# Performance work log

Measured on AMD Instinct MI355X. Metric: run time of the kernel, lower is better.

## Reference

```python
import jax, jax.numpy as jnp
import numpy as np

B, N, INDIM = 512, 200, 200
D1, D2, D3 = 32, 32, 8
RATIO = 0.5
K1 = int(np.ceil(RATIO * N))    # 100 nodes kept after pool1
K2 = int(np.ceil(RATIO * K1))   # 50 nodes kept after pool2
BN_EPS = 1e-5
NEG = -1e9


def setup_inputs() -> dict:
    key = jax.random.key(0)
    ks = jax.random.split(key, 16)
    x = jax.random.normal(ks[0], (B, N, INDIM), jnp.float32)
    u = jax.random.uniform(ks[1], (B, N, N), jnp.float32)
    ut = jnp.triu(jnp.where(u > 0.9, u, 0.0), 1)
    adj = ut + jnp.swapaxes(ut, 1, 2)
    g = lambda i, shape: jax.random.normal(ks[i], shape, jnp.float32) * 0.1
    return dict(
        x=x, adj=adj,
        W1=g(2, (INDIM, D1)), a1s=g(3, (D1,)), a1d=g(4, (D1,)), b1=jnp.zeros((D1,), jnp.float32),
        W2=g(5, (D1, D2)), a2s=g(6, (D2,)), a2d=g(7, (D2,)), b2=jnp.zeros((D2,), jnp.float32),
        pw1=g(8, (D1,)), pw2=g(9, (D2,)),
        fc1_w=g(10, ((D1 + D2) * 2, D2)), fc1_b=jnp.zeros((D2,), jnp.float32),
        fc2_w=g(11, (D2, D3)), fc2_b=jnp.zeros((D3,), jnp.float32),
        fc3_w=g(12, (D3, 2)), fc3_b=jnp.zeros((2,), jnp.float32),
        bn4_g=jnp.ones((D2,), jnp.float32), bn4_b=jnp.zeros((D2,), jnp.float32),
        bn5_g=jnp.ones((D3,), jnp.float32), bn5_b=jnp.zeros((D3,), jnp.float32))


def _gat(x, mask, W, a_s, a_d, b):
    # PyG GATConv (heads=1): alpha_ij = softmax_j LeakyReLU(a_d.h_i + a_s.h_j) over in-neighbors j (self-loops added)
    h = jnp.einsum('bnf,fd->bnd', x, W)
    es = h @ a_s                    # [B,n] source term
    ed = h @ a_d                    # [B,n] dest term
    m = mask | jnp.eye(mask.shape[1], dtype=bool)
    logits = jax.nn.leaky_relu(ed[:, :, None] + es[:, None, :], 0.2)
    alpha = jax.nn.softmax(jnp.where(m, logits, NEG), axis=-1)   # [B,n,n]
    return jnp.einsum('bij,bjd->bid', alpha, h) + b


def _topk(x, adj_w, w, k):
    # TopKPooling(multiplier=1, nonlinearity=sigmoid): score = sigmoid(x.w/||w||)
    score = jax.nn.sigmoid((x @ w) / (jnp.linalg.norm(w) + 1e-16))   # [B,n]
    vals, idx = jax.lax.top_k(score, k)                              # perm sorted desc, as PyG
    xk = jnp.take_along_axis(x, idx[:, :, None], axis=1) * vals[:, :, None]
    ak = jnp.take_along_axis(jnp.take_along_axis(adj_w, idx[:, :, None], axis=1), idx[:, None, :], axis=2)
    return xk, ak, vals


def _bn(z, g, b):
    # eval-mode BatchNorm1d: running_mean=0, running_var=1
    return g * z / jnp.sqrt(1.0 + BN_EPS) + b


def reference(x, adj, W1, a1s, a1d, b1, W2, a2s, a2d, b2, pw1, pw2,
              fc1_w, fc1_b, fc2_w, fc2_b, fc3_w, fc3_b, bn4_g, bn4_b, bn5_g, bn5_b):
    h = _gat(x, adj > 0, W1, a1s, a1d, b1)
    h, aw, s1 = _topk(h, adj, pw1, K1)
    x1 = jnp.concatenate([h.max(axis=1), h.mean(axis=1)], axis=1)    # [B, 64]
    # augment_adj: add self-loops, spspmm (A+I)@(A+I), remove self-loops
    eye = jnp.eye(K1, dtype=aw.dtype)
    a2 = jnp.einsum('bij,bjk->bik', aw + eye, aw + eye) * (1.0 - eye)
    h = _gat(h, a2 != 0, W2, a2s, a2d, b2)
    h, _, s2 = _topk(h, a2, pw2, K2)
    x2 = jnp.concatenate([h.max(axis=1), h.mean(axis=1)], axis=1)    # [B, 64]
    z = jnp.concatenate([x1, x2], axis=1)                            # [B, 128]
    z = _bn(jax.nn.relu(z @ fc1_w + fc1_b), bn4_g, bn4_b)            # dropout: eval -> identity
    z = _bn(jax.nn.relu(z @ fc2_w + fc2_b), bn5_g, bn5_b)
    logp = jax.nn.log_softmax(z @ fc3_w + fc3_b, axis=-1)            # [B, 2]
    return logp, s1, s2
```

## Files before the change

### kernel.cpp

```cpp
#include <hip/hip_runtime.h>
#include <math.h>

#define N_   200
#define B_   512
#define K1_  100
#define K2_  50

#define S1_OFF 1024
#define S2_OFF 52224

#define WS_H    0u
#define WS_ES   13107200u
#define WS_ED   13516800u
#define WS_BITS 13926400u

__device__ __forceinline__ float lrelu(float v) { return v > 0.f ? v : 0.2f * v; }
__device__ __forceinline__ float sigm(float v)  { return 1.f / (1.f + __expf(-v)); }

__device__ __forceinline__ void bitonic_desc(float* key, int* idx, int n, int t) {
  for (int k = 2; k <= n; k <<= 1) {
    for (int j = k >> 1; j > 0; j >>= 1) {
      __syncthreads();
      int ixj = t ^ j;
      if (t < n && ixj > t) {
        float a = key[t], c = key[ixj];
        int ia = idx[t], ic = idx[ixj];
        bool gt = (a > c) || (a == c && ia < ic);
        if (((t & k) == 0) ? !gt : gt) {
          key[t] = c; key[ixj] = a; idx[t] = ic; idx[ixj] = ia;
        }
      }
    }
  }
  __syncthreads();
}

__global__ __launch_bounds__(128) void prep(
    const float* __restrict__ x, const float* __restrict__ adj,
    const float* __restrict__ W1, const float* __restrict__ a1s,
    const float* __restrict__ a1d,
    float* __restrict__ hg, float* __restrict__ esg, float* __restrict__ edg,
    unsigned* __restrict__ bitsg)
{
  const int t = threadIdx.x;
  const int blk = blockIdx.x;
  if (blk < 800) {
    const int r = blk * 128 + t;
    const float* xr = x + (size_t)r * 200;
    float acc[32];
    #pragma unroll
    for (int d = 0; d < 32; ++d) acc[d] = 0.f;
    for (int k4 = 0; k4 < 50; ++k4) {
      float4 xv = *(const float4*)(xr + k4 * 4);
      #pragma unroll
      for (int kk = 0; kk < 4; ++kk) {
        float xs = (&xv.x)[kk];
        const float* wr = W1 + (k4 * 4 + kk) * 32;
        #pragma unroll
        for (int d = 0; d < 32; ++d) acc[d] += xs * wr[d];
      }
    }
    float es = 0.f, ed = 0.f;
    #pragma unroll
    for (int d = 0; d < 32; ++d) { es += acc[d] * a1s[d]; ed += acc[d] * a1d[d]; }
    esg[r] = es; edg[r] = ed;
    float4* hg4 = (float4*)(hg + (size_t)r * 32);
    #pragma unroll
    for (int q = 0; q < 8; ++q)
      hg4[q] = make_float4(acc[q*4], acc[q*4+1], acc[q*4+2], acc[q*4+3]);
  } else {
    const int wg = (blk - 800) * 128 + t;
    const int row = wg / 7;
    const int w = wg - row * 7;
    const float* p = adj + (size_t)row * 200 + w * 32;
    unsigned m = 0u;
    const int lim = (w < 6) ? 32 : 8;
    for (int e = 0; e < lim; e += 4) {
      float4 v = *(const float4*)(p + e);
      m |= (unsigned)(v.x > 0.f) << e;
      m |= (unsigned)(v.y > 0.f) << (e + 1);
      m |= (unsigned)(v.z > 0.f) << (e + 2);
      m |= (unsigned)(v.w > 0.f) << (e + 3);
    }
    bitsg[wg] = m;
  }
}

__global__ __launch_bounds__(256) void gnn_main(
    const float* __restrict__ hg, const float* __restrict__ esg,
    const float* __restrict__ edg, const unsigned* __restrict__ bitsg,
    const float* __restrict__ b1, const float* __restrict__ W2g,
    const float* __restrict__ a2s, const float* __restrict__ a2d,
    const float* __restrict__ b2,
    const float* __restrict__ pw1, const float* __restrict__ pw2,
    const float* __restrict__ fc1w, const float* __restrict__ fc1b,
    const float* __restrict__ fc2w, const float* __restrict__ fc2b,
    const float* __restrict__ fc3w, const float* __restrict__ fc3b,
    const float* __restrict__ bn4g, const float* __restrict__ bn4b,
    const float* __restrict__ bn5g, const float* __restrict__ bn5b,
    float* __restrict__ out)
{
  __shared__ __align__(16) char smem[50592];
  float*    sH    = (float*)smem;
  unsigned* sBITS = (unsigned*)(smem + 25600);
  float*    sW2   = (float*)(smem + 25600);
  float*    sXK   = (float*)(smem + 31200);
  float*    sES   = (float*)(smem + 44000);
  float*    sED   = (float*)(smem + 44800);
  float*    sKey  = (float*)(smem + 45600);
  int*      sIdx  = (int*)(smem + 46624);
  int*      sInv  = (int*)(smem + 46624);
  int*      sSel  = (int*)(smem + 47648);
  float*    sVal  = (float*)(smem + 48048);
  float*    sXV   = (float*)(smem + 48448);
  float*    sRed  = (float*)(smem + 48960);
  unsigned* sMask2= (unsigned*)(smem + 48992);

  const int t = threadIdx.x;
  const int b = blockIdx.x;

  {
    const float4* hsrc = (const float4*)(hg + (size_t)b * 6400);
    float4* hdst = (float4*)sH;
    for (int i = t; i < 1600; i += 256) hdst[i] = hsrc[i];
    if (t < 50) {
      ((float4*)sES)[t] = ((const float4*)(esg + b * 200))[t];
      ((float4*)sED)[t] = ((const float4*)(edg + b * 200))[t];
    }
    const uint4* bsrc = (const uint4*)(bitsg + b * 1400);
    uint4* bdst = (uint4*)sBITS;
    for (int i = t; i < 350; i += 256) bdst[i] = bsrc[i];
  }
  __syncthreads();

  {
    float v = (t < N_) ? sES[t] : -3.0e38f;
    #pragma unroll
    for (int off = 1; off < 64; off <<= 1) v = fmaxf(v, __shfl_xor(v, off, 64));
    if ((t & 63) == 0) sRed[t >> 6] = v;
  }
  __syncthreads();
  const float esmax = fmaxf(fmaxf(sRed[0], sRed[1]), fmaxf(sRed[2], sRed[3]));

  const int wv = t >> 6, lane = t & 63;
  const int dg = lane >> 4, rg = lane & 15;
  float h1v[4][8]; float ssum1[4]; float edv1[4], Lv1[4];
  int rowc1[4]; bool val1[4];
  float b1c[8];
  *(float4*)&b1c[0] = *(const float4*)(b1 + dg * 8);
  *(float4*)&b1c[4] = *(const float4*)(b1 + dg * 8 + 4);
  {
    const int rbase = wv * 50;
    #pragma unroll
    for (int rr = 0; rr < 4; ++rr) {
      int rl = rg + 16 * rr;
      val1[rr] = rl < 50;
      rowc1[rr] = val1[rr] ? (rbase + rl) : 0;
      edv1[rr] = sED[rowc1[rr]];
      Lv1[rr]  = lrelu(edv1[rr] + esmax);
      ssum1[rr] = 0.f;
      #pragma unroll
      for (int u = 0; u < 8; ++u) h1v[rr][u] = 0.f;
    }
    for (int jw = 0; jw < 7; ++jw) {
      unsigned mw[4];
      #pragma unroll
      for (int rr = 0; rr < 4; ++rr) {
        mw[rr] = val1[rr] ? sBITS[rowc1[rr] * 7 + jw] : 0u;
        if (val1[rr] && (rowc1[rr] >> 5) == jw) mw[rr] |= 1u << (rowc1[rr] & 31);
      }
      const int cnt = (jw < 6) ? 32 : 8;
      for (int jj4 = 0; jj4 < cnt; jj4 += 4) {
        float4 esv = *(const float4*)&sES[jw * 32 + jj4];
        #pragma unroll
        for (int u = 0; u < 4; ++u) {
          int jj = jj4 + u;
          int j = jw * 32 + jj;
          float esj = (&esv.x)[u];
          float4 h0 = *(const float4*)&sH[j * 32 + dg * 8];
          float4 h1x = *(const float4*)&sH[j * 32 + dg * 8 + 4];
          #pragma unroll
          for (int rr = 0; rr < 4; ++rr) {
            float w = ((mw[rr] >> jj) & 1u) ? __expf(lrelu(edv1[rr] + esj) - Lv1[rr]) : 0.f;
            ssum1[rr] += w;
            h1v[rr][0] += w * h0.x;  h1v[rr][1] += w * h0.y;
            h1v[rr][2] += w * h0.z;  h1v[rr][3] += w * h0.w;
            h1v[rr][4] += w * h1x.x; h1v[rr][5] += w * h1x.y;
            h1v[rr][6] += w * h1x.z; h1v[rr][7] += w * h1x.w;
          }
        }
      }
    }
    #pragma unroll
    for (int rr = 0; rr < 4; ++rr) {
      float inv = 1.f / ssum1[rr];
      #pragma unroll
      for (int u = 0; u < 8; ++u) h1v[rr][u] = h1v[rr][u] * inv + b1c[u];
    }
  }

  {
    float npw = 0.f;
    #pragma unroll
    for (int d = 0; d < 32; ++d) npw += pw1[d] * pw1[d];
    npw = sqrtf(npw) + 1e-16f;
    float pwc[8];
    *(float4*)&pwc[0] = *(const float4*)(pw1 + dg * 8);
    *(float4*)&pwc[4] = *(const float4*)(pw1 + dg * 8 + 4);
    sKey[t] = -1.f; sIdx[t] = t;
    __syncthreads();
    #pragma unroll
    for (int rr = 0; rr < 4; ++rr) {
      float p = 0.f;
      #pragma unroll
      for (int u = 0; u < 8; ++u) p += h1v[rr][u] * pwc[u];
      p += __shfl_xor(p, 16, 64);
      p += __shfl_xor(p, 32, 64);
      if (dg == 0 && val1[rr]) sKey[rowc1[rr]] = sigm(p / npw);
    }
  }
  bitonic_desc(sKey, sIdx, 256, t);
  if (t < K1_) {
    out[S1_OFF + b * K1_ + t] = sKey[t];
    sVal[t] = sKey[t]; sSel[t] = sIdx[t];
  }
  __syncthreads();
  if (t < 200) sInv[t] = -1;
  __syncthreads();
  if (t < K1_) sInv[sSel[t]] = t;
  __syncthreads();
  #pragma unroll
  for (int rr = 0; rr < 4; ++rr) {
    if (val1[rr]) {
      int rk = sInv[rowc1[rr]];
      if (rk >= 0) {
        float vm = sVal[rk];
        float4 o0 = make_float4(h1v[rr][0]*vm, h1v[rr][1]*vm, h1v[rr][2]*vm, h1v[rr][3]*vm);
        float4 o1 = make_float4(h1v[rr][4]*vm, h1v[rr][5]*vm, h1v[rr][6]*vm, h1v[rr][7]*vm);
        *(float4*)&sXK[rk * 32 + dg * 8]     = o0;
        *(float4*)&sXK[rk * 32 + dg * 8 + 4] = o1;
      }
    }
  }
  __syncthreads();

  if (t < 32) {
    float m = -3.0e38f, s = 0.f;
    for (int r = 0; r < K1_; ++r) { float v = sXK[r * 32 + t]; m = fmaxf(m, v); s += v; }
    sXV[t] = m; sXV[32 + t] = s / 100.f;
  }

  if (t < K1_) {
    int gi = sSel[t];
    unsigned bt[7];
    #pragma unroll
    for (int w = 0; w < 7; ++w) bt[w] = sBITS[gi * 7 + w];
    #pragma unroll
    for (int w = 0; w < 4; ++w) {
      unsigned m = 0;
      const int lim = (w < 3) ? 32 : 4;
      for (int jj = 0; jj < lim; ++jj) {
        int j = w * 32 + jj;
        int gj = sSel[j];
        unsigned bit = (bt[gj >> 5] >> (gj & 31)) & 1u;
        if (j == t) bit = 1u;
        m |= bit << jj;
      }
      sMask2[t * 4 + w] = m;
    }
  }
  __syncthreads();
  {
    unsigned pr0 = 0, pr1 = 0, pr2 = 0, pr3 = 0;
    unsigned ow0 = 0, ow1 = 0, ow2 = 0, ow3 = 0;
    if (t < K1_) {
      ow0 = sMask2[t * 4 + 0]; ow1 = sMask2[t * 4 + 1];
      ow2 = sMask2[t * 4 + 2]; ow3 = sMask2[t * 4 + 3];
    }
    for (int k = 0; k < K1_; ++k) {
      uint4 mk = *(const uint4*)&sMask2[k * 4];
      unsigned bit = (k < 32) ? (ow0 >> k) : (k < 64) ? (ow1 >> (k - 32))
                   : (k < 96) ? (ow2 >> (k - 64)) : (ow3 >> (k - 96));
      unsigned sel = (bit & 1u) ? 0xFFFFFFFFu : 0u;
      pr0 |= mk.x & sel; pr1 |= mk.y & sel; pr2 |= mk.z & sel; pr3 |= mk.w & sel;
    }
    __syncthreads();
    if (t < K1_) {
      sMask2[t * 4 + 0] = pr0; sMask2[t * 4 + 1] = pr1;
      sMask2[t * 4 + 2] = pr2; sMask2[t * 4 + 3] = pr3;
    }
  }
  __syncthreads();

  for (int i = t; i < 1024; i += 256) sW2[i] = W2g[i];
  __syncthreads();
  if (t < K1_) {
    float acc[32];
    #pragma unroll
    for (int d = 0; d < 32; ++d) acc[d] = 0.f;
    const float4* xk4 = (const float4*)(sXK + t * 32);
    for (int k4 = 0; k4 < 8; ++k4) {
      float4 xv = xk4[k4];
      #pragma unroll
      for (int kk = 0; kk < 4; ++kk) {
        float xs = (&xv.x)[kk];
        const float* wr = &sW2[(k4 * 4 + kk) * 32];
        #pragma unroll
        for (int d = 0; d < 32; ++d) acc[d] += xs * wr[d];
      }
    }
    float es = 0.f, ed = 0.f;
    #pragma unroll
    for (int d = 0; d < 32; ++d) { es += acc[d] * a2s[d]; ed += acc[d] * a2d[d]; }
    sES[t] = es; sED[t] = ed;
    #pragma unroll
    for (int d = 0; d < 32; d += 4)
      *(float4*)&sH[t * 32 + d] = make_float4(acc[d], acc[d+1], acc[d+2], acc[d+3]);
  }
  __syncthreads();
  {
    float v = (t < K1_) ? sES[t] : -3.0e38f;
    #pragma unroll
    for (int off = 1; off < 64; off <<= 1) v = fmaxf(v, __shfl_xor(v, off, 64));
    if ((t & 63) == 0) sRed[t >> 6] = v;
  }
  __syncthreads();
  const float esm2 = fmaxf(fmaxf(sRed[0], sRed[1]), fmaxf(sRed[2], sRed[3]));

  float h2v[2][8]; float ssum2[2]; float edv2[2], Lv2[2];
  int rowc2[2]; bool val2[2];
  float b2c[8];
  *(float4*)&b2c[0] = *(const float4*)(b2 + dg * 8);
  *(float4*)&b2c[4] = *(const float4*)(b2 + dg * 8 + 4);
  {
    const int rbase = wv * 25;
    #pragma unroll
    for (int rr = 0; rr < 2; ++rr) {
      int rl = rg + 16 * rr;
      val2[rr] = rl < 25;
      rowc2[rr] = val2[rr] ? (rbase + rl) : 0;
      edv2[rr] = sED[rowc2[rr]];
      Lv2[rr]  = lrelu(edv2[rr] + esm2);
      ssum2[rr] = 0.f;
      #pragma unroll
      for (int u = 0; u < 8; ++u) h2v[rr][u] = 0.f;
    }
    for (int jw = 0; jw < 4; ++jw) {
      unsigned mw[2];
      #pragma unroll
      for (int rr = 0; rr < 2; ++rr)
        mw[rr] = val2[rr] ? sMask2[rowc2[rr] * 4 + jw] : 0u;
      const int cnt = (jw < 3) ? 32 : 4;
      for (int jj4 = 0; jj4 < cnt; jj4 += 4) {
        float4 esv = *(const float4*)&sES[jw * 32 + jj4];
        #pragma unroll
        for (int u = 0; u < 4; ++u) {
          int jj = jj4 + u;
          int j = jw * 32 + jj;
          float esj = (&esv.x)[u];
          float4 h0 = *(const float4*)&sH[j * 32 + dg * 8];
          float4 h1x = *(const float4*)&sH[j * 32 + dg * 8 + 4];
          #pragma unroll
          for (int rr = 0; rr < 2; ++rr) {
            float w = ((mw[rr] >> jj) & 1u) ? __expf(lrelu(edv2[rr] + esj) - Lv2[rr]) : 0.f;
            ssum2[rr] += w;
            h2v[rr][0] += w * h0.x;  h2v[rr][1] += w * h0.y;
            h2v[rr][2] += w * h0.z;  h2v[rr][3] += w * h0.w;
            h2v[rr][4] += w * h1x.x; h2v[rr][5] += w * h1x.y;
            h2v[rr][6] += w * h1x.z; h2v[rr][7] += w * h1x.w;
          }
        }
      }
    }
    #pragma unroll
    for (int rr = 0; rr < 2; ++rr) {
      float inv = 1.f / ssum2[rr];
      #pragma unroll
      for (int u = 0; u < 8; ++u) h2v[rr][u] = h2v[rr][u] * inv + b2c[u];
    }
  }

  {
    float npw = 0.f;
    #pragma unroll
    for (int d = 0; d < 32; ++d) npw += pw2[d] * pw2[d];
    npw = sqrtf(npw) + 1e-16f;
    float pwc[8];
    *(float4*)&pwc[0] = *(const float4*)(pw2 + dg * 8);
    *(float4*)&pwc[4] = *(const float4*)(pw2 + dg * 8 + 4);
    if (t < 128) { sKey[t] = -1.f; sIdx[t] = t; }
    __syncthreads();
    #pragma unroll
    for (int rr = 0; rr < 2; ++rr) {
      float p = 0.f;
      #pragma unroll
      for (int u = 0; u < 8; ++u) p += h2v[rr][u] * pwc[u];
      p += __shfl_xor(p, 16, 64);
      p += __shfl_xor(p, 32, 64);
      if (dg == 0 && val2[rr]) sKey[rowc2[rr]] = sigm(p / npw);
    }
  }
  bitonic_desc(sKey, sIdx, 128, t);
  if (t < K2_) {
    out[S2_OFF + b * K2_ + t] = sKey[t];
    sVal[t] = sKey[t]; sSel[t] = sIdx[t];
  }
  __syncthreads();
  if (t < K1_) sInv[t] = -1;
  __syncthreads();
  if (t < K2_) sInv[sSel[t]] = t;
  __syncthreads();
  #pragma unroll
  for (int rr = 0; rr < 2; ++rr) {
    if (val2[rr]) {
      int rk = sInv[rowc2[rr]];
      if (rk >= 0) {
        float vm = sVal[rk];
        float4 o0 = make_float4(h2v[rr][0]*vm, h2v[rr][1]*vm, h2v[rr][2]*vm, h2v[rr][3]*vm);
        float4 o1 = make_float4(h2v[rr][4]*vm, h2v[rr][5]*vm, h2v[rr][6]*vm, h2v[rr][7]*vm);
        *(float4*)&sXK[rk * 32 + dg * 8]     = o0;
        *(float4*)&sXK[rk * 32 + dg * 8 + 4] = o1;
      }
    }
  }
  __syncthreads();
  if (t < 32) {
    float m = -3.0e38f, s = 0.f;
    for (int r = 0; r < K2_; ++r) { float v = sXK[r * 32 + t]; m = fmaxf(m, v); s += v; }
    sXV[64 + t] = m; sXV[96 + t] = s / 50.f;
  }
  __syncthreads();

  const float RS = 0.99999500003749969f;
  if (t < 32) {
    float z = fc1b[t];
    for (int k = 0; k < 128; ++k) z += sXV[k] * fc1w[k * 32 + t];
    z = fmaxf(z, 0.f);
    z = bn4g[t] * z * RS + bn4b[t];
    sKey[t] = z;
  }
  __syncthreads();
  if (t < 8) {
    float z = fc2b[t];
    for (int k = 0; k < 32; ++k) z += sKey[k] * fc2w[k * 8 + t];
    z = fmaxf(z, 0.f);
    z = bn5g[t] * z * RS + bn5b[t];
    sKey[32 + t] = z;
  }
  __syncthreads();
  if (t < 2) {
    float z = fc3b[t];
    for (int k = 0; k < 8; ++k) z += sKey[32 + k] * fc3w[k * 2 + t];
    sKey[40 + t] = z;
  }
  __syncthreads();
  if (t < 2) {
    float z0 = sKey[40], z1 = sKey[41];
    float m = fmaxf(z0, z1);
    float lse = m + logf(__expf(z0 - m) + __expf(z1 - m));
    out[b * 2 + t] = sKey[40 + t] - lse;
  }
}

extern "C" void kernel_launch(void* const* d_in, const int* in_sizes, int n_in,
                              void* d_out, int out_size, void* d_ws, size_t ws_size,
                              hipStream_t stream) {
  (void)in_sizes; (void)n_in; (void)ws_size; (void)out_size;
  const float* x    = (const float*)d_in[0];
  const float* adj  = (const float*)d_in[1];
  const float* W1   = (const float*)d_in[2];
  const float* a1s  = (const float*)d_in[3];
  const float* a1d  = (const float*)d_in[4];
  const float* b1   = (const float*)d_in[5];
  const float* W2   = (const float*)d_in[6];
  const float* a2s  = (const float*)d_in[7];
  const float* a2d  = (const float*)d_in[8];
  const float* b2   = (const float*)d_in[9];
  const float* pw1  = (const float*)d_in[10];
  const float* pw2  = (const float*)d_in[11];
  const float* fc1w = (const float*)d_in[12];
  const float* fc1b = (const float*)d_in[13];
  const float* fc2w = (const float*)d_in[14];
  const float* fc2b = (const float*)d_in[15];
  const float* fc3w = (const float*)d_in[16];
  const float* fc3b = (const float*)d_in[17];
  const float* bn4g = (const float*)d_in[18];
  const float* bn4b = (const float*)d_in[19];
  const float* bn5g = (const float*)d_in[20];
  const float* bn5b = (const float*)d_in[21];

  char* ws = (char*)d_ws;
  float*    hg    = (float*)(ws + WS_H);
  float*    esg   = (float*)(ws + WS_ES);
  float*    edg   = (float*)(ws + WS_ED);
  unsigned* bitsg = (unsigned*)(ws + WS_BITS);

  prep<<<6400, 128, 0, stream>>>(x, adj, W1, a1s, a1d, hg, esg, edg, bitsg);
  gnn_main<<<B_, 256, 0, stream>>>(hg, esg, edg, bitsg,
                                   b1, W2, a2s, a2d, b2, pw1, pw2,
                                   fc1w, fc1b, fc2w, fc2b, fc3w, fc3b,
                                   bn4g, bn4b, bn5g, bn5b, (float*)d_out);
}
```

Measured before the change: 397.3 us.

## Split prep into separate bitmask and LDS-staged GEMM kernels

The combined prep kernel is split into two launches: one that builds the adjacency bitmask, and one that computes the x·W1 projection. In the projection kernel, each block stages 64 rows of x into shared memory with coalesced float4 loads, and each wavefront computes half of the 32 output columns. The per-wave partial attention dot products are then reduced through LDS. This replaces strided per-thread row reads from global memory, halves register accumulators per thread, and raises parallelism, at the cost of an extra kernel launch and about 51KB of LDS per block, which limits occupancy.

```diff
diff --git a/kernel.cpp b/kernel.cpp
--- a/kernel.cpp
+++ b/kernel.cpp
@@ -35,55 +35,82 @@
   __syncthreads();
 }
 
-__global__ __launch_bounds__(128) void prep(
-    const float* __restrict__ x, const float* __restrict__ adj,
-    const float* __restrict__ W1, const float* __restrict__ a1s,
-    const float* __restrict__ a1d,
-    float* __restrict__ hg, float* __restrict__ esg, float* __restrict__ edg,
-    unsigned* __restrict__ bitsg)
+__global__ __launch_bounds__(128) void prep_gemm(
+    const float* __restrict__ x, const float* __restrict__ W1,
+    const float* __restrict__ a1s, const float* __restrict__ a1d,
+    float* __restrict__ hg, float* __restrict__ esg, float* __restrict__ edg)
 {
+  __shared__ __align__(16) float sX[64 * 200];
+  __shared__ float sP[128];
+  __shared__ float sQ[128];
   const int t = threadIdx.x;
-  const int blk = blockIdx.x;
-  if (blk < 800) {
-    const int r = blk * 128 + t;
-    const float* xr = x + (size_t)r * 200;
-    float acc[32];
-    #pragma unroll
-    for (int d = 0; d < 32; ++d) acc[d] = 0.f;
-    for (int k4 = 0; k4 < 50; ++k4) {
-      float4 xv = *(const float4*)(xr + k4 * 4);
-      #pragma unroll
-      for (int kk = 0; kk < 4; ++kk) {
-        float xs = (&xv.x)[kk];
-        const float* wr = W1 + (k4 * 4 + kk) * 32;
-        #pragma unroll
-        for (int d = 0; d < 32; ++d) acc[d] += xs * wr[d];
-      }
-    }
-    float es = 0.f, ed = 0.f;
-    #pragma unroll
-    for (int d = 0; d < 32; ++d) { es += acc[d] * a1s[d]; ed += acc[d] * a1d[d]; }
-    esg[r] = es; edg[r] = ed;
-    float4* hg4 = (float4*)(hg + (size_t)r * 32);
-    #pragma unroll
-    for (int q = 0; q < 8; ++q)
+  const int r0 = blockIdx.x * 64;
+
+  {
+    const float4* src = (const float4*)(x + (size_t)r0 * 200);
+    float4* dst = (float4*)sX;
+    #pragma unroll
+    for (int i = 0; i < 25; ++i) dst[t + i * 128] = src[t + i * 128];
+  }
+  __syncthreads();
+
+  const int wvu = __builtin_amdgcn_readfirstlane(t >> 6);
+  const int lane = t & 63;
+  const int r = r0 + lane;
+
+  float acc[16];
+  #pragma unroll
+  for (int d = 0; d < 16; ++d) acc[d] = 0.f;
+  const float4* xr4 = (const float4*)(sX + lane * 200);
+  const float* W1h = W1 + wvu * 16;
+  for (int k4 = 0; k4 < 50; ++k4) {
+    float4 xv = xr4[k4];
+    #pragma unroll
+    for (int kk = 0; kk < 4; ++kk) {
+      float xs = (&xv.x)[kk];
+      const float* wr = W1h + (k4 * 4 + kk) * 32;
+      #pragma unroll
+      for (int d = 0; d < 16; ++d) acc[d] += xs * wr[d];
+    }
+  }
+  {
+    float4* hg4 = (float4*)(hg + (size_t)r * 32 + wvu * 16);
+    #pragma unroll
+    for (int q = 0; q < 4; ++q)
       hg4[q] = make_float4(acc[q*4], acc[q*4+1], acc[q*4+2], acc[q*4+3]);
-  } else {
-    const int wg = (blk - 800) * 128 + t;
-    const int row = wg / 7;
-    const int w = wg - row * 7;
-    const float* p = adj + (size_t)row * 200 + w * 32;
-    unsigned m = 0u;
-    const int lim = (w < 6) ? 32 : 8;
-    for (int e = 0; e < lim; e += 4) {
-      float4 v = *(const float4*)(p + e);
-      m |= (unsigned)(v.x > 0.f) << e;
-      m |= (unsigned)(v.y > 0.f) << (e + 1);
-      m |= (unsigned)(v.z > 0.f) << (e + 2);
-      m |= (unsigned)(v.w > 0.f) << (e + 3);
-    }
-    bitsg[wg] = m;
-  }
+  }
+  {
+    const float* as = a1s + wvu * 16;
+    const float* ad = a1d + wvu * 16;
+    float pes = 0.f, ped = 0.f;
+    #pragma unroll
+    for (int d = 0; d < 16; ++d) { pes += acc[d] * as[d]; ped += acc[d] * ad[d]; }
+    sP[t] = pes; sQ[t] = ped;
+  }
+  __syncthreads();
+  if (t < 64) {
+    esg[r0 + t] = sP[t] + sP[64 + t];
+    edg[r0 + t] = sQ[t] + sQ[64 + t];
+  }
+}
+
+__global__ __launch_bounds__(256) void prep_bits(
+    const float* __restrict__ adj, unsigned* __restrict__ bitsg)
+{
+  const int wg = blockIdx.x * 256 + threadIdx.x;
+  const int row = wg / 7;
+  const int w = wg - row * 7;
+  const float* p = adj + (size_t)row * 200 + w * 32;
+  unsigned m = 0u;
+  const int lim = (w < 6) ? 32 : 8;
+  for (int e = 0; e < lim; e += 4) {
+    float4 v = *(const float4*)(p + e);
+    m |= (unsigned)(v.x > 0.f) << e;
+    m |= (unsigned)(v.y > 0.f) << (e + 1);
+    m |= (unsigned)(v.z > 0.f) << (e + 2);
+    m |= (unsigned)(v.w > 0.f) << (e + 3);
+  }
+  bitsg[wg] = m;
 }
 
 __global__ __launch_bounds__(256) void gnn_main(
@@ -495,7 +522,8 @@
   float*    edg   = (float*)(ws + WS_ED);
   unsigned* bitsg = (unsigned*)(ws + WS_BITS);
 
-  prep<<<6400, 128, 0, stream>>>(x, adj, W1, a1s, a1d, hg, esg, edg, bitsg);
+  prep_bits<<<2800, 256, 0, stream>>>(adj, bitsg);
+  prep_gemm<<<1600, 128, 0, stream>>>(x, W1, a1s, a1d, hg, esg, edg);
   gnn_main<<<B_, 256, 0, stream>>>(hg, esg, edg, bitsg,
                                    b1, W2, a2s, a2d, b2, pw1, pw2,
                                    fc1w, fc1b, fc2w, fc2b, fc3w, fc3b,
```

Result: no change. 403.3 us (+1.5%).
